# Kernel optimization log

Measured on AMD Instinct MI355X. Metric: run time of the kernel, lower is better.

## Reference

```python
import jax, jax.numpy as jnp
import numpy as np

NEG = -1e9


def setup_inputs() -> dict:
    key = jax.random.key(0)
    kq, kk, kv, ke = jax.random.split(key, 4)
    B, H, S, D = 4, 16, 2048, 64
    q = jax.random.normal(kq, (B, H, S, D), dtype=jnp.float32)
    k = jax.random.normal(kk, (B, H, S, D), dtype=jnp.float32)
    v = jax.random.normal(kv, (B, H, S, D), dtype=jnp.float32)
    event_length = jax.random.randint(ke, (B,), 0, S, dtype=jnp.int32)
    return {"q": q, "k": k, "v": v, "event_length": event_length}


def reference(q, k, v, event_length):
    B, H, S, D = q.shape
    scale = jnp.sqrt(jnp.asarray(D, dtype=jnp.float32))
    # [b,h,s,q] scores
    scores = jnp.einsum('bhsd,bhqd->bhsq', q, k) / scale
    idx = jnp.arange(S)
    el = event_length[:, None]  # [B,1]
    valid = idx[None, :] < el   # [B,S]
    # mask[b,s,q] = valid[b,s] & valid[b,q]; broadcast over heads
    mask = (valid[:, None, :, None] & valid[:, None, None, :])  # [B,1,S,S]
    scores = jnp.where(mask, scores, NEG)
    attn = jax.nn.softmax(scores, axis=-1)
    # dropout p=0.0 (eval): identity
    out = jnp.einsum('bhsq,bhqd->bhsd', attn, v)
    return out
```

## Files before the change

kernel.cpp:

```cpp
#include <hip/hip_runtime.h>
#include <hip/hip_bf16.h>


#define SQ 2048
#define DH 64
#define NBH 64
#define TK 64
#define NTILE 32
#define TILE_B 8192
#define LDE 72
#define LVP 68

typedef __attribute__((ext_vector_type(4))) float f32x4;
typedef __attribute__((ext_vector_type(8))) short bf16x8;
typedef __attribute__((ext_vector_type(4))) unsigned int u32x4;
typedef __attribute__((ext_vector_type(2))) unsigned int u32x2;

#define VMCNT(n) asm volatile("s_waitcnt vmcnt(" #n ")" ::: "memory")
#define RAW_BARRIER() asm volatile("s_barrier" ::: "memory")

__device__ __forceinline__ unsigned int pk2(float lo, float hi) {
    __hip_bfloat162 h = __float22bfloat162_rn(float2{lo, hi});
    union { __hip_bfloat162 h; unsigned int u; } c; c.h = h;
    return c.u;
}

__device__ __forceinline__ float bfu16_to_f(unsigned short s) {
    union { unsigned int u; float f; } c; c.u = ((unsigned int)s) << 16;
    return c.f;
}

__device__ __forceinline__ void async_cp16(const void* g, void* l) {
    __builtin_amdgcn_global_load_lds(
        (const __attribute__((address_space(1))) unsigned int*)g,
        (__attribute__((address_space(3))) unsigned int*)l, 16, 0, 0);
}


__global__ __launch_bounds__(256)
void convkv(const float* __restrict__ K, const float* __restrict__ V,
            const int* __restrict__ EL, float* __restrict__ MV,
            char* __restrict__ Kbt, char* __restrict__ Vbt) {
    const int bh = blockIdx.x >> 5;
    const int kt = blockIdx.x & 31;
    const int k0 = kt * TK;
    const int el = EL[bh >> 4];
    const int t = threadIdx.x;
    const int r  = t >> 2;
    const int dc = t & 3;

    __shared__ short LV[64][LVP];

    {
        const float* vp = V + ((size_t)bh * SQ + k0 + r) * DH + dc * 16;
        f32x4 a = *(const f32x4*)vp;
        f32x4 b = *(const f32x4*)(vp + 4);
        f32x4 c2 = *(const f32x4*)(vp + 8);
        f32x4 d2 = *(const f32x4*)(vp + 12);
        u32x4 w0, w1;
        w0[0] = pk2(a[0], a[1]);  w0[1] = pk2(a[2], a[3]);
        w0[2] = pk2(b[0], b[1]);  w0[3] = pk2(b[2], b[3]);
        w1[0] = pk2(c2[0], c2[1]); w1[1] = pk2(c2[2], c2[3]);
        w1[2] = pk2(d2[0], d2[1]); w1[3] = pk2(d2[2], d2[3]);
        *(u32x4*)&LV[r][dc * 16]     = w0;
        *(u32x4*)&LV[r][dc * 16 + 8] = w1;
    }

    if (k0 < el) {
        const float* kp = K + ((size_t)bh * SQ + k0 + r) * DH + dc * 16;
        f32x4 a = *(const f32x4*)kp;
        f32x4 b = *(const f32x4*)(kp + 4);
        f32x4 c2 = *(const f32x4*)(kp + 8);
        f32x4 d2 = *(const f32x4*)(kp + 12);
        u32x4 w0, w1;
        w0[0] = pk2(a[0], a[1]);  w0[1] = pk2(a[2], a[3]);
        w0[2] = pk2(b[0], b[1]);  w0[3] = pk2(b[2], b[3]);
        w1[0] = pk2(c2[0], c2[1]); w1[1] = pk2(c2[2], c2[3]);
        w1[2] = pk2(d2[0], d2[1]); w1[3] = pk2(d2[2], d2[3]);
        char* kb = Kbt + (size_t)(bh * NTILE + kt) * TILE_B;
        const int fi  = (r >> 4) * 2 + (dc >> 1);
        const int qd0 = (dc & 1) * 2;
        char* d0 = kb + fi * 1024 + qd0 * 256 + (r & 15) * 16;
        *(u32x4*)d0         = w0;
        *(u32x4*)(d0 + 256) = w1;
    }

    __syncthreads();

    const int dd  = t >> 2;
    const int seg = t & 3;
    float msum = 0.f;
    unsigned int wv[8];
    #pragma unroll
    for (int i = 0; i < 8; ++i) {
        const int pos = seg * 16 + 2 * i;
        const int key = (pos & ~31) | ((pos & 4) << 2) | ((pos & 24) >> 1) | (pos & 3);
        const unsigned short s0 = (unsigned short)LV[key][dd];
        const unsigned short s1 = (unsigned short)LV[key + 1][dd];
        msum += bfu16_to_f(s0) + bfu16_to_f(s1);
        wv[i] = (unsigned int)s0 | ((unsigned int)s1 << 16);
    }
    msum += __shfl_xor(msum, 1);
    msum += __shfl_xor(msum, 2);
    if (seg == 0) atomicAdd(&MV[bh * DH + dd], msum * (1.0f / (float)SQ));

    if (k0 < el) {
        char* vbb = Vbt + (size_t)(bh * NTILE + kt) * TILE_B;
        const int fi  = (seg >> 1) * 4 + (dd >> 4);
        const int qd0 = (seg & 1) * 2;
        char* d0 = vbb + fi * 1024 + qd0 * 256 + (dd & 15) * 16;
        u32x4 o0 = {wv[0], wv[1], wv[2], wv[3]};
        u32x4 o1 = {wv[4], wv[5], wv[6], wv[7]};
        *(u32x4*)d0         = o0;
        *(u32x4*)(d0 + 256) = o1;
    }
}

__global__ __launch_bounds__(512, 4)
void flash13(const float* __restrict__ Q, const int* __restrict__ EL,
             const float* __restrict__ MV, float* __restrict__ O,
             const char* __restrict__ Kbt, const char* __restrict__ Vbt,
             int* __restrict__ ticket) {
    const int t = threadIdx.x;

    {
        const int bh0 = blockIdx.x & (NBH - 1);
        const int qb0 = (blockIdx.x >> 6) * 256;
        const int elb = EL[bh0 >> 4];
        if (qb0 >= elb) {
            float* Op = O + (size_t)bh0 * SQ * DH;
            const int c16 = t & 15, r0 = t >> 4;
            f32x4 mv = *(const f32x4*)(MV + bh0 * DH + c16 * 4);
            #pragma unroll
            for (int i = 0; i < 8; ++i)
                *(f32x4*)(Op + (size_t)(qb0 + r0 + i * 32) * DH + c16 * 4) = mv;
        }
    }

    int ka0 = EL[0], va0 = 0;
    int ka1 = EL[1], va1 = 1;
    int ka2 = EL[2], va2 = 2;
    int ka3 = EL[3], va3 = 3;
    #define CSWAP(x, y) if (ka##x < ka##y) { int tk_ = ka##x, tv_ = va##x; \
        ka##x = ka##y; va##x = va##y; ka##y = tk_; va##y = tv_; }
    CSWAP(0, 1) CSWAP(2, 3) CSWAP(0, 2) CSWAP(1, 3) CSWAP(1, 2)
    #undef CSWAP
    const int c0 = 2 * ((ka0 + 255) >> 8);
    const int c1 = 2 * ((ka1 + 255) >> 8);
    const int c2 = 2 * ((ka2 + 255) >> 8);
    const int c3 = 2 * ((ka3 + 255) >> 8);
    const int nvalid = c0 + c1 + c2 + c3;

    __shared__ char KB[3 * TILE_B];
    __shared__ char VB[3 * TILE_B];
    __shared__ int item_s;

    const int grp = blockIdx.x & 7;
    const int wq = t >> 6, lane = t & 63, qd = lane >> 4, c = lane & 15;
    const float sc = 0.125f * 1.44269504f;

    for (;;) {
        if (t == 0) item_s = atomicAdd(&ticket[grp], 1);
        __syncthreads();
        const int it = item_s;
        if (it >= nvalid) break;

        int u = it, b, el;
        if (u < c0)             { b = va0; el = ka0; }
        else { u -= c0;
        if (u < c1)             { b = va1; el = ka1; }
        else { u -= c1;
        if (u < c2)             { b = va2; el = ka2; }
        else { u -= c2;           b = va3; el = ka3; } } }
        const int vb_ = (el + 255) >> 8;
        const int hh  = u / vb_;
        const int qt  = u - hh * vb_;
        const int bh  = b * 16 + grp + hh * 8;
        const int qbase = qt * 256;

        const float* Qp = Q + (size_t)bh * SQ * DH;
        float*       Op = O + (size_t)bh * SQ * DH;
        const char*  Kt = Kbt + (size_t)bh * NTILE * TILE_B + t * 16;
        const char*  Vt = Vbt + (size_t)bh * NTILE * TILE_B + t * 16;
        char* const  kdst = KB + wq * 1024;
        char* const  vdst = VB + wq * 1024;

        const int nkt = (el + TK - 1) >> 6;

        async_cp16(Kt, kdst);
        async_cp16(Vt, vdst);
        if (nkt > 1) {
            async_cp16(Kt + TILE_B, kdst + TILE_B);
            async_cp16(Vt + TILE_B, vdst + TILE_B);
        }

        bf16x8 qf[2][2];
        #pragma unroll
        for (int nt = 0; nt < 2; ++nt) {
            const int row = qbase + wq * 32 + nt * 16 + c;
            #pragma unroll
            for (int kc = 0; kc < 2; ++kc) {
                const float* p = Qp + (size_t)row * DH + kc * 32 + qd * 8;
                f32x4 a  = *(const f32x4*)p;
                f32x4 bq = *(const f32x4*)(p + 4);
                u32x4 f;
                f[0] = pk2(a[0] * sc, a[1] * sc);
                f[1] = pk2(a[2] * sc, a[3] * sc);
                f[2] = pk2(bq[0] * sc, bq[1] * sc);
                f[3] = pk2(bq[2] * sc, bq[3] * sc);
                qf[nt][kc] = *(bf16x8*)&f;
            }
        }

        float l_[2] = {0.f, 0.f};
        f32x4 oacc[4][2];
        #pragma unroll
        for (int dt = 0; dt < 4; ++dt) {
            oacc[dt][0] = (f32x4){0.f, 0.f, 0.f, 0.f};
            oacc[dt][1] = (f32x4){0.f, 0.f, 0.f, 0.f};
        }

        for (int kt = 0; kt < nkt; ++kt) {
            const int s = kt % 3;

            RAW_BARRIER();
            if (kt + 2 < nkt) {
                const int s2 = (kt + 2) % 3;
                async_cp16(Kt + (size_t)(kt + 2) * TILE_B, kdst + s2 * TILE_B);
                async_cp16(Vt + (size_t)(kt + 2) * TILE_B, vdst + s2 * TILE_B);
            }
            if      (kt + 2 < nkt) VMCNT(4);
            else if (kt + 1 < nkt) VMCNT(2);
            else                   VMCNT(0);
            RAW_BARRIER();

            const char* Kb = KB + s * TILE_B + lane * 16;
            const char* Vb = VB + s * TILE_B + lane * 16;

            f32x4 st[4][2];
            __builtin_amdgcn_s_setprio(1);
            #pragma unroll
            for (int mt = 0; mt < 4; ++mt) {
                bf16x8 a0 = *(const bf16x8*)(Kb + (mt * 2) * 1024);
                bf16x8 a1 = *(const bf16x8*)(Kb + (mt * 2 + 1) * 1024);
                #pragma unroll
                for (int nt = 0; nt < 2; ++nt) {
                    f32x4 acc = (f32x4){0.f, 0.f, 0.f, 0.f};
                    acc = __builtin_amdgcn_mfma_f32_16x16x32_bf16(a0, qf[nt][0], acc, 0, 0, 0);
                    acc = __builtin_amdgcn_mfma_f32_16x16x32_bf16(a1, qf[nt][1], acc, 0, 0, 0);
                    st[mt][nt] = acc;
                }
            }
            __builtin_amdgcn_s_setprio(0);

            const int k0 = kt * TK;
            if (k0 + TK > el) {
                #pragma unroll
                for (int mt = 0; mt < 4; ++mt)
                    #pragma unroll
                    for (int r = 0; r < 4; ++r)
                        if (k0 + mt * 16 + qd * 4 + r >= el) {
                            st[mt][0][r] = -1e30f;
                            st[mt][1][r] = -1e30f;
                        }
            }

            u32x4 pw[2][2];
            #pragma unroll
            for (int nt = 0; nt < 2; ++nt) {
                #pragma unroll
                for (int mt = 0; mt < 4; ++mt) {
                    const float p0 = __builtin_amdgcn_exp2f(st[mt][nt][0]);
                    const float p1 = __builtin_amdgcn_exp2f(st[mt][nt][1]);
                    const float p2 = __builtin_amdgcn_exp2f(st[mt][nt][2]);
                    const float p3 = __builtin_amdgcn_exp2f(st[mt][nt][3]);
                    l_[nt] += (p0 + p1) + (p2 + p3);
                    pw[nt][mt >> 1][(mt & 1) * 2]     = pk2(p0, p1);
                    pw[nt][mt >> 1][(mt & 1) * 2 + 1] = pk2(p2, p3);
                }
            }

            __builtin_amdgcn_s_setprio(1);
            #pragma unroll
            for (int kc = 0; kc < 2; ++kc) {
                bf16x8 pb0 = *(bf16x8*)&pw[0][kc];
                bf16x8 pb1 = *(bf16x8*)&pw[1][kc];
                #pragma unroll
                for (int dt = 0; dt < 4; ++dt) {
                    bf16x8 vf = *(const bf16x8*)(Vb + (kc * 4 + dt) * 1024);
                    oacc[dt][0] = __builtin_amdgcn_mfma_f32_16x16x32_bf16(vf, pb0, oacc[dt][0], 0, 0, 0);
                    oacc[dt][1] = __builtin_amdgcn_mfma_f32_16x16x32_bf16(vf, pb1, oacc[dt][1], 0, 0, 0);
                }
            }
            __builtin_amdgcn_s_setprio(0);
        }

        #pragma unroll
        for (int nt = 0; nt < 2; ++nt) {
            l_[nt] += __shfl_xor(l_[nt], 16);
            l_[nt] += __shfl_xor(l_[nt], 32);
        }

        #pragma unroll
        for (int nt = 0; nt < 2; ++nt) {
            const int qrow = qbase + wq * 32 + nt * 16 + c;
            if (qrow < el) {
                const float inv = 1.0f / l_[nt];
                #pragma unroll
                for (int dt = 0; dt < 4; ++dt) {
                    f32x4 o = oacc[dt][nt];
                    o[0] *= inv; o[1] *= inv; o[2] *= inv; o[3] *= inv;
                    *(f32x4*)(Op + (size_t)qrow * DH + dt * 16 + qd * 4) = o;
                }
            } else {
                #pragma unroll
                for (int dt = 0; dt < 4; ++dt)
                    *(f32x4*)(Op + (size_t)qrow * DH + dt * 16 + qd * 4) =
                        *(const f32x4*)(MV + bh * DH + dt * 16 + qd * 4);
            }
        }
    }
}


__global__ __launch_bounds__(256)
void meanv_k(const float* __restrict__ V, float* __restrict__ MV) {
    const int bh  = blockIdx.x >> 4;
    const int seg = blockIdx.x & 15;
    const float* vp = V + ((size_t)bh * SQ + (size_t)seg * 128) * DH;
    const int c = threadIdx.x & 15;
    const int r = threadIdx.x >> 4;
    const float* p = vp + (size_t)r * DH + c * 4;
    f32x4 s0 = *(const f32x4*)(p);
    f32x4 s1 = *(const f32x4*)(p + 16 * DH);
    f32x4 s2 = *(const f32x4*)(p + 32 * DH);
    f32x4 s3 = *(const f32x4*)(p + 48 * DH);
    s0 += *(const f32x4*)(p + 64 * DH);
    s1 += *(const f32x4*)(p + 80 * DH);
    s2 += *(const f32x4*)(p + 96 * DH);
    s3 += *(const f32x4*)(p + 112 * DH);
    f32x4 s = (s0 + s1) + (s2 + s3);
    __shared__ f32x4 red[16][16];
    red[r][c] = s;
    __syncthreads();
    if (threadIdx.x < 16) {
        f32x4 a = red[0][threadIdx.x];
        #pragma unroll
        for (int j = 1; j < 16; ++j) a += red[j][threadIdx.x];
        const float inv = 1.0f / (float)SQ;
        atomicAdd(&MV[bh * DH + threadIdx.x * 4 + 0], a[0] * inv);
        atomicAdd(&MV[bh * DH + threadIdx.x * 4 + 1], a[1] * inv);
        atomicAdd(&MV[bh * DH + threadIdx.x * 4 + 2], a[2] * inv);
        atomicAdd(&MV[bh * DH + threadIdx.x * 4 + 3], a[3] * inv);
    }
}

__global__ __launch_bounds__(256, 3)
void flash5(const float* __restrict__ Q, const float* __restrict__ K,
            const float* __restrict__ V, const int* __restrict__ EL,
            const float* __restrict__ MV, float* __restrict__ O,
            int* __restrict__ ticket) {
    const int t = threadIdx.x;
    {
        const int bh0    = blockIdx.x & (NBH - 1);
        const int qbase0 = (blockIdx.x >> 6) * 128;
        const int elb    = EL[bh0 >> 4];
        if (qbase0 >= elb) {
            float* Op = O + (size_t)bh0 * SQ * DH;
            const int c16 = t & 15, r0 = t >> 4;
            f32x4 mv = *(const f32x4*)(MV + bh0 * DH + c16 * 4);
            #pragma unroll
            for (int i = 0; i < 8; ++i)
                *(f32x4*)(Op + (size_t)(qbase0 + r0 + i * 16) * DH + c16 * 4) = mv;
        }
    }

    const int el0 = EL[0], el1 = EL[1], el2 = EL[2], el3 = EL[3];
    const int v0 = (el0 + 127) >> 7, v1 = (el1 + 127) >> 7;
    const int v2 = (el2 + 127) >> 7, v3 = (el3 + 127) >> 7;
    const int n0 = 16 * v0, n1 = n0 + 16 * v1, n2 = n1 + 16 * v2;
    const int nvalid = n2 + 16 * v3;

    __shared__ short Kb[TK][LDE];
    __shared__ short Vt[DH][LDE];
    __shared__ short Pl[4][32][LDE];
    __shared__ int item_s;

    const int wq = t >> 6, lane = t & 63, qd = lane >> 4, c = lane & 15;
    const int ksrow = t >> 2;
    const int ksdc  = t & 3;
    const int vpair = t & 31;
    const int vdg   = t >> 5;

    for (;;) {
        if (t == 0) item_s = atomicAdd(ticket, 1);
        __syncthreads();
        const int it = item_s;
        if (it >= nvalid) break;

        int b, u, vb, el;
        if      (it < n0) { b = 0; u = it;      vb = v0; el = el0; }
        else if (it < n1) { b = 1; u = it - n0; vb = v1; el = el1; }
        else if (it < n2) { b = 2; u = it - n1; vb = v2; el = el2; }
        else              { b = 3; u = it - n2; vb = v3; el = el3; }
        const int head  = u / vb;
        const int qt    = u - head * vb;
        const int bh    = b * 16 + head;
        const int qbase = qt * 128;

        const size_t base = (size_t)bh * SQ * DH;
        const float* Qp = Q + base;
        const float* Kp = K + base;
        const float* Vp = V + base;
        float* Op = O + base;

        const float sc = 0.125f * 1.44269504f;
        bf16x8 qf[2][2];
        #pragma unroll
        for (int nt = 0; nt < 2; ++nt) {
            const int row = qbase + wq * 32 + nt * 16 + c;
            #pragma unroll
            for (int kc = 0; kc < 2; ++kc) {
                const float* p = Qp + (size_t)row * DH + kc * 32 + qd * 8;
                f32x4 a  = *(const f32x4*)p;
                f32x4 bb = *(const f32x4*)(p + 4);
                u32x4 f;
                f[0] = pk2(a[0] * sc, a[1] * sc);
                f[1] = pk2(a[2] * sc, a[3] * sc);
                f[2] = pk2(bb[0] * sc, bb[1] * sc);
                f[3] = pk2(bb[2] * sc, bb[3] * sc);
                qf[nt][kc] = *(bf16x8*)&f;
            }
        }

        float l_[2] = {0.f, 0.f};
        f32x4 oacc[4][2];
        #pragma unroll
        for (int dt = 0; dt < 4; ++dt)
            #pragma unroll
            for (int nt = 0; nt < 2; ++nt)
                oacc[dt][nt] = (f32x4){0.f, 0.f, 0.f, 0.f};

        const int nkt = (el + TK - 1) / TK;

        f32x4 kg0, kg1, kg2, kg3, vg0, vg1, vg2, vg3;
        {
            const float* kp = Kp + (size_t)ksrow * DH + ksdc * 16;
            kg0 = *(const f32x4*)kp;
            kg1 = *(const f32x4*)(kp + 4);
            kg2 = *(const f32x4*)(kp + 8);
            kg3 = *(const f32x4*)(kp + 12);
            const float* vp0 = Vp + (size_t)(2 * vpair) * DH + vdg * 8;
            vg0 = *(const f32x4*)vp0;
            vg1 = *(const f32x4*)(vp0 + 4);
            vg2 = *(const f32x4*)(vp0 + DH);
            vg3 = *(const f32x4*)(vp0 + DH + 4);
        }

        for (int kt = 0; kt < nkt; ++kt) {
            const int k0 = kt * TK;

            __syncthreads();
            {
                u32x4 w0, w1;
                w0[0] = pk2(kg0[0], kg0[1]); w0[1] = pk2(kg0[2], kg0[3]);
                w0[2] = pk2(kg1[0], kg1[1]); w0[3] = pk2(kg1[2], kg1[3]);
                w1[0] = pk2(kg2[0], kg2[1]); w1[1] = pk2(kg2[2], kg2[3]);
                w1[2] = pk2(kg3[0], kg3[1]); w1[3] = pk2(kg3[2], kg3[3]);
                *(u32x4*)&Kb[ksrow][ksdc * 16]     = w0;
                *(u32x4*)&Kb[ksrow][ksdc * 16 + 8] = w1;
            }
            {
                #pragma unroll
                for (int i = 0; i < 4; ++i) {
                    *(unsigned int*)&Vt[vdg * 8 + i][2 * vpair]     = pk2(vg0[i], vg2[i]);
                    *(unsigned int*)&Vt[vdg * 8 + 4 + i][2 * vpair] = pk2(vg1[i], vg3[i]);
                }
            }
            __syncthreads();

            if (kt + 1 < nkt) {
                const int kn = k0 + TK;
                const float* kp = Kp + (size_t)(kn + ksrow) * DH + ksdc * 16;
                kg0 = *(const f32x4*)kp;
                kg1 = *(const f32x4*)(kp + 4);
                kg2 = *(const f32x4*)(kp + 8);
                kg3 = *(const f32x4*)(kp + 12);
                const float* vp0 = Vp + (size_t)(kn + 2 * vpair) * DH + vdg * 8;
                vg0 = *(const f32x4*)vp0;
                vg1 = *(const f32x4*)(vp0 + 4);
                vg2 = *(const f32x4*)(vp0 + DH);
                vg3 = *(const f32x4*)(vp0 + DH + 4);
            }

            f32x4 st[4][2];
            #pragma unroll
            for (int mt = 0; mt < 4; ++mt) {
                bf16x8 a0 = *(const bf16x8*)&Kb[mt * 16 + c][qd * 8];
                bf16x8 a1 = *(const bf16x8*)&Kb[mt * 16 + c][32 + qd * 8];
                #pragma unroll
                for (int nt = 0; nt < 2; ++nt) {
                    f32x4 acc = (f32x4){0.f, 0.f, 0.f, 0.f};
                    acc = __builtin_amdgcn_mfma_f32_16x16x32_bf16(a0, qf[nt][0], acc, 0, 0, 0);
                    acc = __builtin_amdgcn_mfma_f32_16x16x32_bf16(a1, qf[nt][1], acc, 0, 0, 0);
                    st[mt][nt] = acc;
                }
            }

            if (k0 + TK > el) {
                #pragma unroll
                for (int mt = 0; mt < 4; ++mt)
                    #pragma unroll
                    for (int r = 0; r < 4; ++r)
                        if (k0 + mt * 16 + qd * 4 + r >= el) {
                            st[mt][0][r] = -1e30f;
                            st[mt][1][r] = -1e30f;
                        }
            }

            #pragma unroll
            for (int nt = 0; nt < 2; ++nt) {
                #pragma unroll
                for (int mt = 0; mt < 4; ++mt) {
                    const float p0 = exp2f(st[mt][nt][0]);
                    const float p1 = exp2f(st[mt][nt][1]);
                    const float p2 = exp2f(st[mt][nt][2]);
                    const float p3 = exp2f(st[mt][nt][3]);
                    l_[nt] += (p0 + p1) + (p2 + p3);
                    u32x2 pw;
                    pw[0] = pk2(p0, p1);
                    pw[1] = pk2(p2, p3);
                    *(u32x2*)&Pl[wq][nt * 16 + c][mt * 16 + qd * 4] = pw;
                }
            }

            #pragma unroll
            for (int kc = 0; kc < 2; ++kc) {
                bf16x8 pb0 = *(const bf16x8*)&Pl[wq][c][kc * 32 + qd * 8];
                bf16x8 pb1 = *(const bf16x8*)&Pl[wq][16 + c][kc * 32 + qd * 8];
                #pragma unroll
                for (int dt = 0; dt < 4; ++dt) {
                    bf16x8 vf = *(const bf16x8*)&Vt[dt * 16 + c][kc * 32 + qd * 8];
                    oacc[dt][0] = __builtin_amdgcn_mfma_f32_16x16x32_bf16(vf, pb0, oacc[dt][0], 0, 0, 0);
                    oacc[dt][1] = __builtin_amdgcn_mfma_f32_16x16x32_bf16(vf, pb1, oacc[dt][1], 0, 0, 0);
                }
            }
        }

        #pragma unroll
        for (int nt = 0; nt < 2; ++nt) {
            l_[nt] += __shfl_xor(l_[nt], 16);
            l_[nt] += __shfl_xor(l_[nt], 32);
        }

        #pragma unroll
        for (int nt = 0; nt < 2; ++nt) {
            const int row = qbase + wq * 32 + nt * 16 + c;
            if (row < el) {
                const float inv = 1.0f / l_[nt];
                #pragma unroll
                for (int dt = 0; dt < 4; ++dt) {
                    f32x4 o = oacc[dt][nt];
                    o[0] *= inv; o[1] *= inv; o[2] *= inv; o[3] *= inv;
                    *(f32x4*)(Op + (size_t)row * DH + dt * 16 + qd * 4) = o;
                }
            } else {
                #pragma unroll
                for (int dt = 0; dt < 4; ++dt) {
                    f32x4 mv = *(const f32x4*)(MV + bh * DH + dt * 16 + qd * 4);
                    *(f32x4*)(Op + (size_t)row * DH + dt * 16 + qd * 4) = mv;
                }
            }
        }
    }
}


extern "C" void kernel_launch(void* const* d_in, const int* in_sizes, int n_in,
                              void* d_out, int out_size, void* d_ws, size_t ws_size,
                              hipStream_t stream) {
    const float* q  = (const float*)d_in[0];
    const float* k  = (const float*)d_in[1];
    const float* v  = (const float*)d_in[2];
    const int*   el = (const int*)d_in[3];
    float* out = (float*)d_out;

    const size_t kbt_bytes = (size_t)NBH * NTILE * TILE_B;
    const size_t needed    = 65536 + 2 * kbt_bytes;

    if (ws_size >= needed) {
        float* mv  = (float*)d_ws;
        int*   tk  = (int*)((char*)d_ws + 16384);
        char*  kbt = (char*)d_ws + 65536;
        char*  vbt = kbt + kbt_bytes;

        hipMemsetAsync(d_ws, 0, 65536, stream);
        convkv<<<dim3(NBH * NTILE), dim3(256), 0, stream>>>(k, v, el, mv, kbt, vbt);
        flash13<<<dim3(NBH * (SQ / 256)), dim3(512), 0, stream>>>(q, el, mv, out, kbt, vbt, tk);
    } else {
        float* mv = (float*)d_ws;
        int*   tk = (int*)((char*)d_ws + NBH * DH * sizeof(float));

        hipMemsetAsync(d_ws, 0, NBH * DH * sizeof(float) + 64, stream);
        meanv_k<<<dim3(NBH * 16), dim3(256), 0, stream>>>(v, mv);
        flash5<<<dim3(NBH * (SQ / 128)), dim3(256), 0, stream>>>(q, k, v, el, mv, out, tk);
    }
}
```

Measured before the change: 192.5 us.

## Shrink flash blocks to 64-row query tiles with double-buffered KV staging

Shrinks the attention kernel from 512-thread blocks covering 256 query rows to 128-thread blocks covering 64 query rows. Work items are now counted per 64-row tile of valid length, which cuts the padded work past event_length. K/V staging changes from a 3-stage ring filled by 8 waves to a 2-stage double buffer, where each thread issues 4 copies per tensor per stage. The pre-fill of masked rows with the mean of V now runs at 64-row granularity. Smaller blocks give finer load balance and less wasted compute, but each K/V tile is reused by fewer query rows, so global/L2 traffic and per-block overhead go up.

New measurement: 190.2 us. Within noise of the previous version (-1.2%).

```diff
diff --git a/kernel.cpp b/kernel.cpp
--- a/kernel.cpp
+++ b/kernel.cpp
@@ -116,8 +116,8 @@
     }
 }
 
-__global__ __launch_bounds__(512, 4)
-void flash13(const float* __restrict__ Q, const int* __restrict__ EL,
+__global__ __launch_bounds__(128, 2)
+void flash14(const float* __restrict__ Q, const int* __restrict__ EL,
              const float* __restrict__ MV, float* __restrict__ O,
              const char* __restrict__ Kbt, const char* __restrict__ Vbt,
              int* __restrict__ ticket) {
@@ -125,15 +125,18 @@
 
     {
         const int bh0 = blockIdx.x & (NBH - 1);
-        const int qb0 = (blockIdx.x >> 6) * 256;
-        const int elb = EL[bh0 >> 4];
-        if (qb0 >= elb) {
+        const int qb0 = (blockIdx.x >> 6) * 128;
+        const int el64b = (EL[bh0 >> 4] + 63) & ~63;
+        if (qb0 + 127 >= el64b) {
             float* Op = O + (size_t)bh0 * SQ * DH;
             const int c16 = t & 15, r0 = t >> 4;
             f32x4 mv = *(const f32x4*)(MV + bh0 * DH + c16 * 4);
             #pragma unroll
-            for (int i = 0; i < 8; ++i)
-                *(f32x4*)(Op + (size_t)(qb0 + r0 + i * 32) * DH + c16 * 4) = mv;
+            for (int i = 0; i < 16; ++i) {
+                const int row = qb0 + r0 + i * 8;
+                if (row >= el64b)
+                    *(f32x4*)(Op + (size_t)row * DH + c16 * 4) = mv;
+            }
         }
     }
 
@@ -145,14 +148,14 @@
         ka##x = ka##y; va##x = va##y; ka##y = tk_; va##y = tv_; }
     CSWAP(0, 1) CSWAP(2, 3) CSWAP(0, 2) CSWAP(1, 3) CSWAP(1, 2)
     #undef CSWAP
-    const int c0 = 2 * ((ka0 + 255) >> 8);
-    const int c1 = 2 * ((ka1 + 255) >> 8);
-    const int c2 = 2 * ((ka2 + 255) >> 8);
-    const int c3 = 2 * ((ka3 + 255) >> 8);
+    const int c0 = 2 * ((ka0 + 63) >> 6);
+    const int c1 = 2 * ((ka1 + 63) >> 6);
+    const int c2 = 2 * ((ka2 + 63) >> 6);
+    const int c3 = 2 * ((ka3 + 63) >> 6);
     const int nvalid = c0 + c1 + c2 + c3;
 
-    __shared__ char KB[3 * TILE_B];
-    __shared__ char VB[3 * TILE_B];
+    __shared__ char KB[2 * TILE_B];
+    __shared__ char VB[2 * TILE_B];
     __shared__ int item_s;
 
     const int grp = blockIdx.x & 7;
@@ -172,32 +175,39 @@
         else { u -= c1;
         if (u < c2)             { b = va2; el = ka2; }
         else { u -= c2;           b = va3; el = ka3; } } }
-        const int vb_ = (el + 255) >> 8;
+        const int vb_ = (el + 63) >> 6;
         const int hh  = u / vb_;
         const int qt  = u - hh * vb_;
         const int bh  = b * 16 + grp + hh * 8;
-        const int qbase = qt * 256;
+        const int qbase = qt * 64;
 
         const float* Qp = Q + (size_t)bh * SQ * DH;
         float*       Op = O + (size_t)bh * SQ * DH;
         const char*  Kt = Kbt + (size_t)bh * NTILE * TILE_B + t * 16;
         const char*  Vt = Vbt + (size_t)bh * NTILE * TILE_B + t * 16;
-        char* const  kdst = KB + wq * 1024;
-        char* const  vdst = VB + wq * 1024;
 
         const int nkt = (el + TK - 1) >> 6;
 
-        async_cp16(Kt, kdst);
-        async_cp16(Vt, vdst);
-        if (nkt > 1) {
-            async_cp16(Kt + TILE_B, kdst + TILE_B);
-            async_cp16(Vt + TILE_B, vdst + TILE_B);
-        }
-
+        #define STAGE(kt_, s_) {                                               \
+            const char* gk_ = Kt + (size_t)(kt_) * TILE_B;                     \
+            const char* gv_ = Vt + (size_t)(kt_) * TILE_B;                     \
+            char* lk_ = KB + (s_) * TILE_B + t * 16;                           \
+            char* lv_ = VB + (s_) * TILE_B + t * 16;                           \
+            _Pragma("unroll")                                                  \
+            for (int j_ = 0; j_ < 4; ++j_)                                     \
+                async_cp16(gk_ + j_ * 2048, lk_ + j_ * 2048);                  \
+            _Pragma("unroll")                                                  \
+            for (int j_ = 0; j_ < 4; ++j_)                                     \
+                async_cp16(gv_ + j_ * 2048, lv_ + j_ * 2048);                  \
+        }
+
+        STAGE(0, 0)
+
+        const int qrow0 = qbase + wq * 32;
         bf16x8 qf[2][2];
         #pragma unroll
         for (int nt = 0; nt < 2; ++nt) {
-            const int row = qbase + wq * 32 + nt * 16 + c;
+            const int row = qrow0 + nt * 16 + c;
             #pragma unroll
             for (int kc = 0; kc < 2; ++kc) {
                 const float* p = Qp + (size_t)row * DH + kc * 32 + qd * 8;
@@ -221,17 +231,11 @@
         }
 
         for (int kt = 0; kt < nkt; ++kt) {
-            const int s = kt % 3;
+            const int s = kt & 1;
 
             RAW_BARRIER();
-            if (kt + 2 < nkt) {
-                const int s2 = (kt + 2) % 3;
-                async_cp16(Kt + (size_t)(kt + 2) * TILE_B, kdst + s2 * TILE_B);
-                async_cp16(Vt + (size_t)(kt + 2) * TILE_B, vdst + s2 * TILE_B);
-            }
-            if      (kt + 2 < nkt) VMCNT(4);
-            else if (kt + 1 < nkt) VMCNT(2);
-            else                   VMCNT(0);
+            if (kt + 1 < nkt) STAGE(kt + 1, s ^ 1)
+            if (kt + 1 < nkt) VMCNT(8); else VMCNT(0);
             RAW_BARRIER();
 
             const char* Kb = KB + s * TILE_B + lane * 16;
@@ -294,6 +298,7 @@
             }
             __builtin_amdgcn_s_setprio(0);
         }
+        #undef STAGE
 
         #pragma unroll
         for (int nt = 0; nt < 2; ++nt) {
@@ -303,7 +308,7 @@
 
         #pragma unroll
         for (int nt = 0; nt < 2; ++nt) {
-            const int qrow = qbase + wq * 32 + nt * 16 + c;
+            const int qrow = qrow0 + nt * 16 + c;
             if (qrow < el) {
                 const float inv = 1.0f / l_[nt];
                 #pragma unroll
@@ -596,7 +601,7 @@
 
         hipMemsetAsync(d_ws, 0, 65536, stream);
         convkv<<<dim3(NBH * NTILE), dim3(256), 0, stream>>>(k, v, el, mv, kbt, vbt);
-        flash13<<<dim3(NBH * (SQ / 256)), dim3(512), 0, stream>>>(q, el, mv, out, kbt, vbt, tk);
+        flash14<<<dim3(NBH * 16), dim3(128), 0, stream>>>(q, el, mv, out, kbt, vbt, tk);
     } else {
         float* mv = (float*)d_ws;
         int*   tk = (int*)((char*)d_ws + NBH * DH * sizeof(float));
```

## Replace atomic work-ticket loop with static block mapping and 128-key double-buffered phases

Applied to the files above, without the earlier changes.

The persistent ticket-based scheduler, which used an atomicAdd per work item plus a block-wide sync, is replaced by a static mapping where each block takes item blockIdx>>3 and blocks with no work exit early. The K/V pipeline changes from a 3-stage ring of 64-key tiles to a 2-stage double buffer of 128-key phases, and each phase processes two 64-key sub-tiles per barrier pair. This halves the number of barriers and removes the atomic round trip, at the cost of larger LDS use per stage and shallower prefetch depth. Static mapping may balance load less well than dynamic tickets.

Result: faster. 186.1 us (-3.3%).

```diff
diff --git a/kernel.cpp b/kernel.cpp
--- a/kernel.cpp
+++ b/kernel.cpp
@@ -8,6 +8,7 @@
 #define TK 64
 #define NTILE 32
 #define TILE_B 8192
+#define PH_B 16384
 #define LDE 72
 #define LVP 68
 
@@ -117,10 +118,9 @@
 }
 
 __global__ __launch_bounds__(512, 4)
-void flash13(const float* __restrict__ Q, const int* __restrict__ EL,
+void flash15(const float* __restrict__ Q, const int* __restrict__ EL,
              const float* __restrict__ MV, float* __restrict__ O,
-             const char* __restrict__ Kbt, const char* __restrict__ Vbt,
-             int* __restrict__ ticket) {
+             const char* __restrict__ Kbt, const char* __restrict__ Vbt) {
     const int t = threadIdx.x;
 
     {
@@ -151,91 +151,90 @@
     const int c3 = 2 * ((ka3 + 255) >> 8);
     const int nvalid = c0 + c1 + c2 + c3;
 
-    __shared__ char KB[3 * TILE_B];
-    __shared__ char VB[3 * TILE_B];
-    __shared__ int item_s;
+    __shared__ char KB[2 * PH_B];
+    __shared__ char VB[2 * PH_B];
 
     const int grp = blockIdx.x & 7;
+    const int it  = blockIdx.x >> 3;
+    if (it >= nvalid) return;
+
+    int u = it, b, el;
+    if (u < c0)             { b = va0; el = ka0; }
+    else { u -= c0;
+    if (u < c1)             { b = va1; el = ka1; }
+    else { u -= c1;
+    if (u < c2)             { b = va2; el = ka2; }
+    else { u -= c2;           b = va3; el = ka3; } } }
+    const int vb_ = (el + 255) >> 8;
+    const int hh  = u / vb_;
+    const int qt  = u - hh * vb_;
+    const int bh  = b * 16 + grp + hh * 8;
+    const int qbase = qt * 256;
+
     const int wq = t >> 6, lane = t & 63, qd = lane >> 4, c = lane & 15;
     const float sc = 0.125f * 1.44269504f;
 
-    for (;;) {
-        if (t == 0) item_s = atomicAdd(&ticket[grp], 1);
-        __syncthreads();
-        const int it = item_s;
-        if (it >= nvalid) break;
-
-        int u = it, b, el;
-        if (u < c0)             { b = va0; el = ka0; }
-        else { u -= c0;
-        if (u < c1)             { b = va1; el = ka1; }
-        else { u -= c1;
-        if (u < c2)             { b = va2; el = ka2; }
-        else { u -= c2;           b = va3; el = ka3; } } }
-        const int vb_ = (el + 255) >> 8;
-        const int hh  = u / vb_;
-        const int qt  = u - hh * vb_;
-        const int bh  = b * 16 + grp + hh * 8;
-        const int qbase = qt * 256;
-
-        const float* Qp = Q + (size_t)bh * SQ * DH;
-        float*       Op = O + (size_t)bh * SQ * DH;
-        const char*  Kt = Kbt + (size_t)bh * NTILE * TILE_B + t * 16;
-        const char*  Vt = Vbt + (size_t)bh * NTILE * TILE_B + t * 16;
-        char* const  kdst = KB + wq * 1024;
-        char* const  vdst = VB + wq * 1024;
-
-        const int nkt = (el + TK - 1) >> 6;
-
-        async_cp16(Kt, kdst);
-        async_cp16(Vt, vdst);
-        if (nkt > 1) {
-            async_cp16(Kt + TILE_B, kdst + TILE_B);
-            async_cp16(Vt + TILE_B, vdst + TILE_B);
-        }
-
-        bf16x8 qf[2][2];
+    const float* Qp = Q + (size_t)bh * SQ * DH;
+    float*       Op = O + (size_t)bh * SQ * DH;
+    const char*  Kt = Kbt + (size_t)bh * NTILE * TILE_B + t * 16;
+    const char*  Vt = Vbt + (size_t)bh * NTILE * TILE_B + t * 16;
+
+    const int nph = (el + 127) >> 7;
+
+    #define STAGE(ph_, s_) {                                                   \
+        const char* gk_ = Kt + (size_t)(ph_) * PH_B;                           \
+        const char* gv_ = Vt + (size_t)(ph_) * PH_B;                           \
+        char* lk_ = KB + (s_) * PH_B + t * 16;                                 \
+        char* lv_ = VB + (s_) * PH_B + t * 16;                                 \
+        async_cp16(gk_,        lk_);                                           \
+        async_cp16(gk_ + 8192, lk_ + 8192);                                    \
+        async_cp16(gv_,        lv_);                                           \
+        async_cp16(gv_ + 8192, lv_ + 8192);                                    \
+    }
+
+    STAGE(0, 0)
+
+    bf16x8 qf[2][2];
+    #pragma unroll
+    for (int nt = 0; nt < 2; ++nt) {
+        const int row = qbase + wq * 32 + nt * 16 + c;
         #pragma unroll
-        for (int nt = 0; nt < 2; ++nt) {
-            const int row = qbase + wq * 32 + nt * 16 + c;
-            #pragma unroll
-            for (int kc = 0; kc < 2; ++kc) {
-                const float* p = Qp + (size_t)row * DH + kc * 32 + qd * 8;
-                f32x4 a  = *(const f32x4*)p;
-                f32x4 bq = *(const f32x4*)(p + 4);
-                u32x4 f;
-                f[0] = pk2(a[0] * sc, a[1] * sc);
-                f[1] = pk2(a[2] * sc, a[3] * sc);
-                f[2] = pk2(bq[0] * sc, bq[1] * sc);
-                f[3] = pk2(bq[2] * sc, bq[3] * sc);
-                qf[nt][kc] = *(bf16x8*)&f;
-            }
-        }
-
-        float l_[2] = {0.f, 0.f};
-        f32x4 oacc[4][2];
+        for (int kc = 0; kc < 2; ++kc) {
+            const float* p = Qp + (size_t)row * DH + kc * 32 + qd * 8;
+            f32x4 a  = *(const f32x4*)p;
+            f32x4 bq = *(const f32x4*)(p + 4);
+            u32x4 f;
+            f[0] = pk2(a[0] * sc, a[1] * sc);
+            f[1] = pk2(a[2] * sc, a[3] * sc);
+            f[2] = pk2(bq[0] * sc, bq[1] * sc);
+            f[3] = pk2(bq[2] * sc, bq[3] * sc);
+            qf[nt][kc] = *(bf16x8*)&f;
+        }
+    }
+
+    float l_[2] = {0.f, 0.f};
+    f32x4 oacc[4][2];
+    #pragma unroll
+    for (int dt = 0; dt < 4; ++dt) {
+        oacc[dt][0] = (f32x4){0.f, 0.f, 0.f, 0.f};
+        oacc[dt][1] = (f32x4){0.f, 0.f, 0.f, 0.f};
+    }
+
+    for (int ph = 0; ph < nph; ++ph) {
+        const int s = ph & 1;
+
+        RAW_BARRIER();
+        if (ph + 1 < nph) STAGE(ph + 1, s ^ 1)
+        if (ph + 1 < nph) VMCNT(4); else VMCNT(0);
+        RAW_BARRIER();
+
         #pragma unroll
-        for (int dt = 0; dt < 4; ++dt) {
-            oacc[dt][0] = (f32x4){0.f, 0.f, 0.f, 0.f};
-            oacc[dt][1] = (f32x4){0.f, 0.f, 0.f, 0.f};
-        }
-
-        for (int kt = 0; kt < nkt; ++kt) {
-            const int s = kt % 3;
-
-            RAW_BARRIER();
-            if (kt + 2 < nkt) {
-                const int s2 = (kt + 2) % 3;
-                async_cp16(Kt + (size_t)(kt + 2) * TILE_B, kdst + s2 * TILE_B);
-                async_cp16(Vt + (size_t)(kt + 2) * TILE_B, vdst + s2 * TILE_B);
-            }
-            if      (kt + 2 < nkt) VMCNT(4);
-            else if (kt + 1 < nkt) VMCNT(2);
-            else                   VMCNT(0);
-            RAW_BARRIER();
-
-            const char* Kb = KB + s * TILE_B + lane * 16;
-            const char* Vb = VB + s * TILE_B + lane * 16;
+        for (int su = 0; su < 2; ++su) {
+            const int k0 = ph * 128 + su * 64;
+            if (k0 >= el) break;
+
+            const char* Kb = KB + s * PH_B + su * TILE_B + lane * 16;
+            const char* Vb = VB + s * PH_B + su * TILE_B + lane * 16;
 
             f32x4 st[4][2];
             __builtin_amdgcn_s_setprio(1);
@@ -253,7 +252,6 @@
             }
             __builtin_amdgcn_s_setprio(0);
 
-            const int k0 = kt * TK;
             if (k0 + TK > el) {
                 #pragma unroll
                 for (int mt = 0; mt < 4; ++mt)
@@ -294,30 +292,31 @@
             }
             __builtin_amdgcn_s_setprio(0);
         }
-
-        #pragma unroll
-        for (int nt = 0; nt < 2; ++nt) {
-            l_[nt] += __shfl_xor(l_[nt], 16);
-            l_[nt] += __shfl_xor(l_[nt], 32);
-        }
-
-        #pragma unroll
-        for (int nt = 0; nt < 2; ++nt) {
-            const int qrow = qbase + wq * 32 + nt * 16 + c;
-            if (qrow < el) {
-                const float inv = 1.0f / l_[nt];
-                #pragma unroll
-                for (int dt = 0; dt < 4; ++dt) {
-                    f32x4 o = oacc[dt][nt];
-                    o[0] *= inv; o[1] *= inv; o[2] *= inv; o[3] *= inv;
-                    *(f32x4*)(Op + (size_t)qrow * DH + dt * 16 + qd * 4) = o;
-                }
-            } else {
-                #pragma unroll
-                for (int dt = 0; dt < 4; ++dt)
-                    *(f32x4*)(Op + (size_t)qrow * DH + dt * 16 + qd * 4) =
-                        *(const f32x4*)(MV + bh * DH + dt * 16 + qd * 4);
-            }
+    }
+    #undef STAGE
+
+    #pragma unroll
+    for (int nt = 0; nt < 2; ++nt) {
+        l_[nt] += __shfl_xor(l_[nt], 16);
+        l_[nt] += __shfl_xor(l_[nt], 32);
+    }
+
+    #pragma unroll
+    for (int nt = 0; nt < 2; ++nt) {
+        const int qrow = qbase + wq * 32 + nt * 16 + c;
+        if (qrow < el) {
+            const float inv = 1.0f / l_[nt];
+            #pragma unroll
+            for (int dt = 0; dt < 4; ++dt) {
+                f32x4 o = oacc[dt][nt];
+                o[0] *= inv; o[1] *= inv; o[2] *= inv; o[3] *= inv;
+                *(f32x4*)(Op + (size_t)qrow * DH + dt * 16 + qd * 4) = o;
+            }
+        } else {
+            #pragma unroll
+            for (int dt = 0; dt < 4; ++dt)
+                *(f32x4*)(Op + (size_t)qrow * DH + dt * 16 + qd * 4) =
+                    *(const f32x4*)(MV + bh * DH + dt * 16 + qd * 4);
         }
     }
 }
@@ -590,13 +589,12 @@
 
     if (ws_size >= needed) {
         float* mv  = (float*)d_ws;
-        int*   tk  = (int*)((char*)d_ws + 16384);
         char*  kbt = (char*)d_ws + 65536;
         char*  vbt = kbt + kbt_bytes;
 
         hipMemsetAsync(d_ws, 0, 65536, stream);
         convkv<<<dim3(NBH * NTILE), dim3(256), 0, stream>>>(k, v, el, mv, kbt, vbt);
-        flash13<<<dim3(NBH * (SQ / 256)), dim3(512), 0, stream>>>(q, el, mv, out, kbt, vbt, tk);
+        flash15<<<dim3(NBH * (SQ / 256)), dim3(512), 0, stream>>>(q, el, mv, out, kbt, vbt);
     } else {
         float* mv = (float*)d_ws;
         int*   tk = (int*)((char*)d_ws + NBH * DH * sizeof(float));
```
